# Optimization experiments

Measured on AMD Instinct MI355X. Metric: run time of the kernel, lower is better.

Reference implementation:

```python
import jax, jax.numpy as jnp
import numpy as np

B, N, D, E, FF, K = 2, 1024, 768, 8, 4, 2
H = D * FF  # 3072


def _xavier_uniform(key, shape, gain=1.0):
    # shape is (..., out, in) like torch Linear weight; fan_in/out from last two dims
    fan_out, fan_in = shape[-2], shape[-1]
    limit = gain * np.sqrt(6.0 / (fan_in + fan_out))
    return jax.random.uniform(key, shape, jnp.float32, -limit, limit)


def setup_inputs() -> dict:
    key = jax.random.key(0)
    ks = jax.random.split(key, 5)
    tokens = jax.random.normal(ks[0], (B, N, D), jnp.float32)
    # Token-choice top-K routing: softmax over experts, keep top-K weights
    logits = jax.random.normal(ks[1], (B, N, E), jnp.float32)
    probs = jax.nn.softmax(logits, axis=-1)
    topv, topi = jax.lax.top_k(probs, K)              # (B,N,K)
    onehot = jax.nn.one_hot(topi, E, dtype=jnp.float32)  # (B,N,K,E)
    combine_weights = jnp.einsum('bnk,bnke->bne', topv, onehot)  # (B,N,E)
    dispatch_weights = (combine_weights > 0).astype(jnp.float32)
    # Stacked expert weights (torch Linear convention: W is (out, in), y = x @ W.T)
    Wg = _xavier_uniform(ks[2], (E, H, D))
    Wv = _xavier_uniform(ks[3], (E, H, D))
    Wo = _xavier_uniform(ks[4], (E, D, H), gain=0.02)
    scale = jnp.full((E,), 1.0 / E, jnp.float32)  # output_scale init = 1/E
    return dict(tokens=tokens, dispatch_weights=dispatch_weights,
                combine_weights=combine_weights, Wg=Wg, Wv=Wv, Wo=Wo, scale=scale)


def reference(tokens, dispatch_weights, combine_weights, Wg, Wv, Wo, scale):
    Bb, Nn, Dd = tokens.shape
    Ee = Wg.shape[0]
    x = tokens.reshape(Bb * Nn, Dd)                    # (T, D)
    mask = (dispatch_weights.reshape(-1, Ee) > 0).astype(x.dtype)  # (T, E)
    comb = combine_weights.reshape(-1, Ee) * mask      # zero where not dispatched
    # SwiGLU-style expert FFN, all experts in one grouped contraction
    gate = jax.nn.gelu(jnp.einsum('td,ehd->teh', x, Wg), approximate=False)  # (T,E,H)
    value = jnp.einsum('td,ehd->teh', x, Wv)           # (T,E,H)
    expert_out = jnp.einsum('teh,edh->ted', gate * value, Wo) * scale[None, :, None]  # (T,E,D)
    # Weighted combine: sum_e comb[t,e] * expert_out[t,e,:]
    y = jnp.einsum('ted,te->td', expert_out, comb)     # (T, D)
    return y.reshape(Bb, Nn, Dd)
```

## Files before the change

### kernel.cpp

```cpp
#include <hip/hip_runtime.h>
#include <hip/hip_bf16.h>
#include <math.h>

#define T_TOK 2048
#define DIM   768
#define NEXP  8
#define HDIM  3072
#define MAXP  (T_TOK * 2)
#define LDST  40
#define NTILE_MAX 40

typedef __attribute__((ext_vector_type(8))) short bfrag;
typedef __attribute__((ext_vector_type(4))) float f32x4;

__device__ __forceinline__ unsigned short f2bf(float f) {
  union { float f; unsigned int u; } x; x.f = f;
  unsigned int r = x.u + 0x7fffu + ((x.u >> 16) & 1u);
  return (unsigned short)(r >> 16);
}

__global__ void k_route(const float* __restrict__ disp,
                        const float* __restrict__ comb,
                        int* __restrict__ meta,
                        float* __restrict__ row_comb,
                        int* __restrict__ row_token,
                        int* __restrict__ tok2pair) {
  __shared__ int s_cnt[NEXP], s_off[NEXP], s_cur[NEXP];
  __shared__ int s_tn[T_TOK];
  int tid = threadIdx.x;
  if (tid < NEXP) s_cnt[tid] = 0;
  for (int t = tid; t < T_TOK; t += 256) s_tn[t] = 0;
  __syncthreads();
  for (int t = tid; t < T_TOK; t += 256)
    for (int e = 0; e < NEXP; ++e)
      if (disp[t * NEXP + e] > 0.f) atomicAdd(&s_cnt[e], 1);
  __syncthreads();
  if (tid == 0) {
    int acc = 0;
    for (int e = 0; e < NEXP; ++e) { s_off[e] = acc; acc += s_cnt[e]; }
  }
  __syncthreads();
  if (tid < NEXP) {
    s_cur[tid] = s_off[tid];
    meta[tid] = s_cnt[tid];
    meta[NEXP + tid] = s_off[tid];
  }
  __syncthreads();
  for (int t = tid; t < T_TOK; t += 256)
    for (int e = 0; e < NEXP; ++e)
      if (disp[t * NEXP + e] > 0.f) {
        int p = atomicAdd(&s_cur[e], 1);
        row_token[p] = t;
        row_comb[p] = comb[t * NEXP + e];
        int sl = atomicAdd(&s_tn[t], 1);
        tok2pair[t * 2 + sl] = p;
      }
  __syncthreads();
  if (tid == 0) {
    int nt = 0;
    for (int e = 0; e < NEXP; ++e)
      for (int m0 = 0; m0 < s_cnt[e]; m0 += 128)
        meta[17 + nt++] = (e << 16) | (m0 >> 7);
    meta[16] = nt;
  }
}

__global__ void k_xbf(const float* __restrict__ X, unsigned short* __restrict__ Xb) {
  size_t i = ((size_t)blockIdx.x * 256 + threadIdx.x) * 8;
  float4 a = *(const float4*)(X + i);
  float4 b = *(const float4*)(X + i + 4);
  unsigned short r[8];
  r[0]=f2bf(a.x); r[1]=f2bf(a.y); r[2]=f2bf(a.z); r[3]=f2bf(a.w);
  r[4]=f2bf(b.x); r[5]=f2bf(b.y); r[6]=f2bf(b.z); r[7]=f2bf(b.w);
  *(uint4*)(Xb + i) = *(uint4*)r;
}

__global__ __launch_bounds__(256, 2) void k_gemm_gv(
    const unsigned short* __restrict__ Xb,
    const float* __restrict__ Wg,
    const float* __restrict__ Wv,
    const int* __restrict__ meta,
    const int* __restrict__ row_token,
    unsigned short* __restrict__ ubuf)
{
  int blk = blockIdx.x;
  int c = blk & 7, slot = blk >> 3;
  int nt = c + 8 * (slot / NTILE_MAX);
  int t  = slot % NTILE_MAX;
  if (t >= meta[16]) return;
  int tv = meta[17 + t];
  int e = tv >> 16, m0 = (tv & 0xffff) << 7;
  int cnt = meta[e], off = meta[NEXP + e];
  int n0 = nt * 128;

  __shared__ unsigned short As[128 * LDST];
  __shared__ unsigned short Bgs[128 * LDST];
  __shared__ unsigned short Bvs[128 * LDST];

  int tid = threadIdx.x;
  int wid = tid >> 6, lane = tid & 63;
  int wm = (wid >> 1) * 64, wn = (wid & 1) * 64;
  int lr = lane & 15, quad = lane >> 4;

  int a_tok[2];
#pragma unroll
  for (int r = 0; r < 2; ++r) {
    int row = (tid + 256 * r) >> 2;
    int gr = m0 + row; if (gr >= cnt) gr = cnt - 1;
    a_tok[r] = row_token[off + gr];
  }

  const float* Wgb = Wg + (size_t)e * ((size_t)HDIM * DIM);
  const float* Wvb = Wv + (size_t)e * ((size_t)HDIM * DIM);

  f32x4 zero4 = {0.f, 0.f, 0.f, 0.f};
  f32x4 accg[4][4], accv[4][4];
#pragma unroll
  for (int i = 0; i < 4; ++i)
#pragma unroll
    for (int j = 0; j < 4; ++j) { accg[i][j] = zero4; accv[i][j] = zero4; }

  for (int k0 = 0; k0 < DIM; k0 += 32) {
    __syncthreads();
#pragma unroll
    for (int r = 0; r < 2; ++r) {
      int c2 = tid + 256 * r;
      int row = c2 >> 2, sub = c2 & 3;
      uint4 av = *(const uint4*)(Xb + (size_t)a_tok[r] * DIM + k0 + sub * 8);
      *(uint4*)(&As[row * LDST + sub * 8]) = av;
    }
#pragma unroll
    for (int r = 0; r < 4; ++r) {
      int c2 = tid + 256 * r;
      int row = c2 >> 3, c4 = c2 & 7;
      float4 gv = *(const float4*)(Wgb + (size_t)(n0 + row) * DIM + k0 + c4 * 4);
      ushort4 gp;
      gp.x = f2bf(gv.x); gp.y = f2bf(gv.y); gp.z = f2bf(gv.z); gp.w = f2bf(gv.w);
      *(ushort4*)(&Bgs[row * LDST + c4 * 4]) = gp;
      float4 vv = *(const float4*)(Wvb + (size_t)(n0 + row) * DIM + k0 + c4 * 4);
      ushort4 vp;
      vp.x = f2bf(vv.x); vp.y = f2bf(vv.y); vp.z = f2bf(vv.z); vp.w = f2bf(vv.w);
      *(ushort4*)(&Bvs[row * LDST + c4 * 4]) = vp;
    }
    __syncthreads();
    bfrag a[4], bg[4], bv[4];
#pragma unroll
    for (int i = 0; i < 4; ++i)
      a[i] = *(const bfrag*)(&As[(wm + i * 16 + lr) * LDST + quad * 8]);
#pragma unroll
    for (int j = 0; j < 4; ++j) {
      bg[j] = *(const bfrag*)(&Bgs[(wn + j * 16 + lr) * LDST + quad * 8]);
      bv[j] = *(const bfrag*)(&Bvs[(wn + j * 16 + lr) * LDST + quad * 8]);
    }
#pragma unroll
    for (int i = 0; i < 4; ++i)
#pragma unroll
      for (int j = 0; j < 4; ++j) {
        accg[i][j] = __builtin_amdgcn_mfma_f32_16x16x32_bf16(a[i], bg[j], accg[i][j], 0, 0, 0);
        accv[i][j] = __builtin_amdgcn_mfma_f32_16x16x32_bf16(a[i], bv[j], accv[i][j], 0, 0, 0);
      }
  }

#pragma unroll
  for (int i = 0; i < 4; ++i)
#pragma unroll
    for (int rg = 0; rg < 4; ++rg) {
      int gr = m0 + wm + i * 16 + quad * 4 + rg;
      if (gr < cnt) {
        size_t base = (size_t)(off + gr) * HDIM + n0 + wn;
#pragma unroll
        for (int j = 0; j < 4; ++j) {
          float g = accg[i][j][rg];
          float v = accv[i][j][rg];
          float u = 0.5f * g * (1.0f + erff(g * 0.70710678118654752f)) * v;
          ubuf[base + j * 16 + lr] = f2bf(u);
        }
      }
    }
}

__global__ __launch_bounds__(256, 2) void k_gemm_out(
    const unsigned short* __restrict__ U,
    const float* __restrict__ Wo,
    const float* __restrict__ scale,
    const int* __restrict__ meta,
    const int* __restrict__ row_token,
    const float* __restrict__ row_comb,
    float* __restrict__ partial,
    float* __restrict__ out,
    int mode)
{
  int blk = blockIdx.x;
  int c = blk & 7, slot = blk >> 3;
  int sidx = c + 8 * (slot / NTILE_MAX);
  int nt = sidx % 6, ks = sidx / 6;
  int t = slot % NTILE_MAX;
  if (t >= meta[16]) return;
  int tv = meta[17 + t];
  int e = tv >> 16, m0 = (tv & 0xffff) << 7;
  int cnt = meta[e], off = meta[NEXP + e];
  int n0 = nt * 128;
  int kbase = ks * (HDIM / 4);

  __shared__ unsigned short As[128 * LDST];
  __shared__ unsigned short Bs[128 * LDST];

  int tid = threadIdx.x;
  int wid = tid >> 6, lane = tid & 63;
  int wm = (wid >> 1) * 64, wn = (wid & 1) * 64;
  int lr = lane & 15, quad = lane >> 4;

  int a_grow[2];
#pragma unroll
  for (int r = 0; r < 2; ++r) {
    int row = (tid + 256 * r) >> 2;
    int gr = m0 + row; if (gr >= cnt) gr = cnt - 1;
    a_grow[r] = off + gr;
  }

  const float* Wb = Wo + (size_t)e * ((size_t)DIM * HDIM);

  f32x4 zero4 = {0.f, 0.f, 0.f, 0.f};
  f32x4 acc[4][4];
#pragma unroll
  for (int i = 0; i < 4; ++i)
#pragma unroll
    for (int j = 0; j < 4; ++j) acc[i][j] = zero4;

  for (int kk = 0; kk < HDIM / 4; kk += 32) {
    int k0 = kbase + kk;
    __syncthreads();
#pragma unroll
    for (int r = 0; r < 2; ++r) {
      int c2 = tid + 256 * r;
      int row = c2 >> 2, sub = c2 & 3;
      uint4 av = *(const uint4*)(U + (size_t)a_grow[r] * HDIM + k0 + sub * 8);
      *(uint4*)(&As[row * LDST + sub * 8]) = av;
    }
#pragma unroll
    for (int r = 0; r < 4; ++r) {
      int c2 = tid + 256 * r;
      int row = c2 >> 3, c4 = c2 & 7;
      float4 bvv = *(const float4*)(Wb + (size_t)(n0 + row) * HDIM + k0 + c4 * 4);
      ushort4 bp;
      bp.x = f2bf(bvv.x); bp.y = f2bf(bvv.y); bp.z = f2bf(bvv.z); bp.w = f2bf(bvv.w);
      *(ushort4*)(&Bs[row * LDST + c4 * 4]) = bp;
    }
    __syncthreads();
    bfrag a[4], b[4];
#pragma unroll
    for (int i = 0; i < 4; ++i)
      a[i] = *(const bfrag*)(&As[(wm + i * 16 + lr) * LDST + quad * 8]);
#pragma unroll
    for (int j = 0; j < 4; ++j)
      b[j] = *(const bfrag*)(&Bs[(wn + j * 16 + lr) * LDST + quad * 8]);
#pragma unroll
    for (int i = 0; i < 4; ++i)
#pragma unroll
      for (int j = 0; j < 4; ++j)
        acc[i][j] = __builtin_amdgcn_mfma_f32_16x16x32_bf16(a[i], b[j], acc[i][j], 0, 0, 0);
  }

  float sc = scale[e];
#pragma unroll
  for (int i = 0; i < 4; ++i)
#pragma unroll
    for (int rg = 0; rg < 4; ++rg) {
      int gr = m0 + wm + i * 16 + quad * 4 + rg;
      if (gr < cnt) {
        int grow = off + gr;
        float w = row_comb[grow] * sc;
        if (mode == 0) {
          float* pb = partial + ((size_t)ks * MAXP + grow) * DIM + n0 + wn;
#pragma unroll
          for (int j = 0; j < 4; ++j)
            pb[j * 16 + lr] = acc[i][j][rg] * w;
        } else {
          int tok = row_token[grow];
          float* ob = out + (size_t)tok * DIM + n0 + wn;
#pragma unroll
          for (int j = 0; j < 4; ++j)
            atomicAdd(ob + j * 16 + lr, acc[i][j][rg] * w);
        }
      }
    }
}

__global__ void k_combine(const float* __restrict__ partial,
                          const int* __restrict__ tok2pair,
                          float* __restrict__ out) {
  int idx = blockIdx.x * 256 + threadIdx.x;
  int t = idx / 192, d4 = idx % 192;
  int p0 = tok2pair[t * 2], p1 = tok2pair[t * 2 + 1];
  float sx = 0.f, sy = 0.f, sz = 0.f, sw = 0.f;
#pragma unroll
  for (int ks = 0; ks < 4; ++ks) {
    float4 a = *(const float4*)(partial + ((size_t)ks * MAXP + p0) * DIM + d4 * 4);
    float4 b = *(const float4*)(partial + ((size_t)ks * MAXP + p1) * DIM + d4 * 4);
    sx += a.x + b.x; sy += a.y + b.y; sz += a.z + b.z; sw += a.w + b.w;
  }
  float4 r; r.x = sx; r.y = sy; r.z = sz; r.w = sw;
  *(float4*)(out + (size_t)t * DIM + d4 * 4) = r;
}

extern "C" void kernel_launch(void* const* d_in, const int* in_sizes, int n_in,
                              void* d_out, int out_size, void* d_ws, size_t ws_size,
                              hipStream_t stream) {
  const float* tokens = (const float*)d_in[0];
  const float* disp   = (const float*)d_in[1];
  const float* comb   = (const float*)d_in[2];
  const float* Wg     = (const float*)d_in[3];
  const float* Wv     = (const float*)d_in[4];
  const float* Wo     = (const float*)d_in[5];
  const float* scale  = (const float*)d_in[6];
  float* out = (float*)d_out;

  char* ws = (char*)d_ws;
  int*   meta      = (int*)ws;
  int*   row_token = (int*)(ws + 16384);
  float* row_comb  = (float*)(ws + 32768);
  int*   tok2pair  = (int*)(ws + 49152);
  unsigned short* Xb   = (unsigned short*)(ws + (1u << 20));
  unsigned short* ubuf = (unsigned short*)(ws + (5u << 20));
  float* partial = (float*)(ws + (32ull << 20));
  size_t need_partial = (32ull << 20) + (size_t)4 * MAXP * DIM * sizeof(float);
  int mode = (ws_size >= need_partial) ? 0 : 1;

  hipLaunchKernelGGL(k_route, dim3(1), dim3(256), 0, stream,
                     disp, comb, meta, row_comb, row_token, tok2pair);
  hipLaunchKernelGGL(k_xbf, dim3((T_TOK * DIM) / (256 * 8)), dim3(256), 0, stream,
                     tokens, Xb);
  hipLaunchKernelGGL(k_gemm_gv, dim3(NTILE_MAX * 24), dim3(256), 0, stream,
                     Xb, Wg, Wv, meta, row_token, ubuf);
  if (mode == 1)
    hipMemsetAsync(d_out, 0, (size_t)out_size * sizeof(float), stream);
  hipLaunchKernelGGL(k_gemm_out, dim3(NTILE_MAX * 6 * 4), dim3(256), 0, stream,
                     ubuf, Wo, scale, meta, row_token, row_comb, partial, out, mode);
  if (mode == 0)
    hipLaunchKernelGGL(k_combine, dim3((T_TOK * DIM / 4) / 256), dim3(256), 0, stream,
                       partial, tok2pair, out);
}
```

Measured before the change: 411.0 us.

## Shrink gate/value GEMM M-tile to 64 and register-prefetch next K slice

The gate/value GEMM now uses 64-row token tiles, with its own 64-row tile list built in the routing kernel, so more blocks are launched and the idle padding rows per expert shrink. Both GEMMs now load the next K slice of activations and weights into registers while the current slice is being consumed, which hides global load latency behind the MFMA work. The cost is more register pressure and, for the smaller tile, each fp32 weight tile is reloaded and converted about twice as often.

```diff
diff --git a/kernel.cpp b/kernel.cpp
--- a/kernel.cpp
+++ b/kernel.cpp
@@ -8,7 +8,8 @@
 #define HDIM  3072
 #define MAXP  (T_TOK * 2)
 #define LDST  40
-#define NTILE_MAX 40
+#define NT64_MAX  72
+#define NT128_MAX 40
 
 typedef __attribute__((ext_vector_type(8))) short bfrag;
 typedef __attribute__((ext_vector_type(4))) float f32x4;
@@ -59,9 +60,14 @@
   if (tid == 0) {
     int nt = 0;
     for (int e = 0; e < NEXP; ++e)
+      for (int m0 = 0; m0 < s_cnt[e]; m0 += 64)
+        meta[17 + nt++] = (e << 16) | (m0 >> 6);
+    meta[16] = nt;
+    int nt2 = 0;
+    for (int e = 0; e < NEXP; ++e)
       for (int m0 = 0; m0 < s_cnt[e]; m0 += 128)
-        meta[17 + nt++] = (e << 16) | (m0 >> 7);
-    meta[16] = nt;
+        meta[90 + nt2++] = (e << 16) | (m0 >> 7);
+    meta[89] = nt2;
   }
 }
 
@@ -85,67 +91,77 @@
 {
   int blk = blockIdx.x;
   int c = blk & 7, slot = blk >> 3;
-  int nt = c + 8 * (slot / NTILE_MAX);
-  int t  = slot % NTILE_MAX;
+  int nt = c + 8 * (slot / NT64_MAX);
+  int t  = slot % NT64_MAX;
   if (t >= meta[16]) return;
   int tv = meta[17 + t];
-  int e = tv >> 16, m0 = (tv & 0xffff) << 7;
+  int e = tv >> 16, m0 = (tv & 0xffff) << 6;
   int cnt = meta[e], off = meta[NEXP + e];
   int n0 = nt * 128;
 
-  __shared__ unsigned short As[128 * LDST];
+  __shared__ unsigned short As[64 * LDST];
   __shared__ unsigned short Bgs[128 * LDST];
   __shared__ unsigned short Bvs[128 * LDST];
 
   int tid = threadIdx.x;
   int wid = tid >> 6, lane = tid & 63;
-  int wm = (wid >> 1) * 64, wn = (wid & 1) * 64;
+  int wm = (wid >> 1) * 32, wn = (wid & 1) * 64;
   int lr = lane & 15, quad = lane >> 4;
 
-  int a_tok[2];
-#pragma unroll
-  for (int r = 0; r < 2; ++r) {
-    int row = (tid + 256 * r) >> 2;
-    int gr = m0 + row; if (gr >= cnt) gr = cnt - 1;
-    a_tok[r] = row_token[off + gr];
-  }
+  int arow = tid >> 2, asub = tid & 3;
+  int atok;
+  { int gr = m0 + arow; if (gr >= cnt) gr = cnt - 1;
+    atok = row_token[off + gr]; }
 
   const float* Wgb = Wg + (size_t)e * ((size_t)HDIM * DIM);
   const float* Wvb = Wv + (size_t)e * ((size_t)HDIM * DIM);
 
+  int brow[4], bc4[4];
+#pragma unroll
+  for (int r = 0; r < 4; ++r) { int c2 = tid + 256 * r; brow[r] = c2 >> 3; bc4[r] = c2 & 7; }
+
   f32x4 zero4 = {0.f, 0.f, 0.f, 0.f};
-  f32x4 accg[4][4], accv[4][4];
-#pragma unroll
-  for (int i = 0; i < 4; ++i)
+  f32x4 accg[2][4], accv[2][4];
+#pragma unroll
+  for (int i = 0; i < 2; ++i)
 #pragma unroll
     for (int j = 0; j < 4; ++j) { accg[i][j] = zero4; accv[i][j] = zero4; }
+
+  uint4 aR;
+  float4 gR[4], vR[4];
+
+  aR = *(const uint4*)(Xb + (size_t)atok * DIM + asub * 8);
+#pragma unroll
+  for (int r = 0; r < 4; ++r) {
+    gR[r] = *(const float4*)(Wgb + (size_t)(n0 + brow[r]) * DIM + bc4[r] * 4);
+    vR[r] = *(const float4*)(Wvb + (size_t)(n0 + brow[r]) * DIM + bc4[r] * 4);
+  }
 
   for (int k0 = 0; k0 < DIM; k0 += 32) {
     __syncthreads();
-#pragma unroll
-    for (int r = 0; r < 2; ++r) {
-      int c2 = tid + 256 * r;
-      int row = c2 >> 2, sub = c2 & 3;
-      uint4 av = *(const uint4*)(Xb + (size_t)a_tok[r] * DIM + k0 + sub * 8);
-      *(uint4*)(&As[row * LDST + sub * 8]) = av;
-    }
+    *(uint4*)(&As[arow * LDST + asub * 8]) = aR;
 #pragma unroll
     for (int r = 0; r < 4; ++r) {
-      int c2 = tid + 256 * r;
-      int row = c2 >> 3, c4 = c2 & 7;
-      float4 gv = *(const float4*)(Wgb + (size_t)(n0 + row) * DIM + k0 + c4 * 4);
       ushort4 gp;
-      gp.x = f2bf(gv.x); gp.y = f2bf(gv.y); gp.z = f2bf(gv.z); gp.w = f2bf(gv.w);
-      *(ushort4*)(&Bgs[row * LDST + c4 * 4]) = gp;
-      float4 vv = *(const float4*)(Wvb + (size_t)(n0 + row) * DIM + k0 + c4 * 4);
+      gp.x = f2bf(gR[r].x); gp.y = f2bf(gR[r].y); gp.z = f2bf(gR[r].z); gp.w = f2bf(gR[r].w);
+      *(ushort4*)(&Bgs[brow[r] * LDST + bc4[r] * 4]) = gp;
       ushort4 vp;
-      vp.x = f2bf(vv.x); vp.y = f2bf(vv.y); vp.z = f2bf(vv.z); vp.w = f2bf(vv.w);
-      *(ushort4*)(&Bvs[row * LDST + c4 * 4]) = vp;
+      vp.x = f2bf(vR[r].x); vp.y = f2bf(vR[r].y); vp.z = f2bf(vR[r].z); vp.w = f2bf(vR[r].w);
+      *(ushort4*)(&Bvs[brow[r] * LDST + bc4[r] * 4]) = vp;
+    }
+    int kn = k0 + 32;
+    if (kn < DIM) {
+      aR = *(const uint4*)(Xb + (size_t)atok * DIM + kn + asub * 8);
+#pragma unroll
+      for (int r = 0; r < 4; ++r) {
+        gR[r] = *(const float4*)(Wgb + (size_t)(n0 + brow[r]) * DIM + kn + bc4[r] * 4);
+        vR[r] = *(const float4*)(Wvb + (size_t)(n0 + brow[r]) * DIM + kn + bc4[r] * 4);
+      }
     }
     __syncthreads();
-    bfrag a[4], bg[4], bv[4];
-#pragma unroll
-    for (int i = 0; i < 4; ++i)
+    bfrag a[2], bg[4], bv[4];
+#pragma unroll
+    for (int i = 0; i < 2; ++i)
       a[i] = *(const bfrag*)(&As[(wm + i * 16 + lr) * LDST + quad * 8]);
 #pragma unroll
     for (int j = 0; j < 4; ++j) {
@@ -153,7 +169,7 @@
       bv[j] = *(const bfrag*)(&Bvs[(wn + j * 16 + lr) * LDST + quad * 8]);
     }
 #pragma unroll
-    for (int i = 0; i < 4; ++i)
+    for (int i = 0; i < 2; ++i)
 #pragma unroll
       for (int j = 0; j < 4; ++j) {
         accg[i][j] = __builtin_amdgcn_mfma_f32_16x16x32_bf16(a[i], bg[j], accg[i][j], 0, 0, 0);
@@ -162,7 +178,7 @@
   }
 
 #pragma unroll
-  for (int i = 0; i < 4; ++i)
+  for (int i = 0; i < 2; ++i)
 #pragma unroll
     for (int rg = 0; rg < 4; ++rg) {
       int gr = m0 + wm + i * 16 + quad * 4 + rg;
@@ -192,11 +208,11 @@
 {
   int blk = blockIdx.x;
   int c = blk & 7, slot = blk >> 3;
-  int sidx = c + 8 * (slot / NTILE_MAX);
+  int sidx = c + 8 * (slot / NT128_MAX);
   int nt = sidx % 6, ks = sidx / 6;
-  int t = slot % NTILE_MAX;
-  if (t >= meta[16]) return;
-  int tv = meta[17 + t];
+  int t = slot % NT128_MAX;
+  if (t >= meta[89]) return;
+  int tv = meta[90 + t];
   int e = tv >> 16, m0 = (tv & 0xffff) << 7;
   int cnt = meta[e], off = meta[NEXP + e];
   int n0 = nt * 128;
@@ -217,8 +233,13 @@
     int gr = m0 + row; if (gr >= cnt) gr = cnt - 1;
     a_grow[r] = off + gr;
   }
+  int asub = tid & 3;
 
   const float* Wb = Wo + (size_t)e * ((size_t)DIM * HDIM);
+
+  int brow[4], bc4[4];
+#pragma unroll
+  for (int r = 0; r < 4; ++r) { int c2 = tid + 256 * r; brow[r] = c2 >> 3; bc4[r] = c2 & 7; }
 
   f32x4 zero4 = {0.f, 0.f, 0.f, 0.f};
   f32x4 acc[4][4];
@@ -226,25 +247,39 @@
   for (int i = 0; i < 4; ++i)
 #pragma unroll
     for (int j = 0; j < 4; ++j) acc[i][j] = zero4;
+
+  uint4 aR[2];
+  float4 bR[4];
+
+#pragma unroll
+  for (int r = 0; r < 2; ++r)
+    aR[r] = *(const uint4*)(U + (size_t)a_grow[r] * HDIM + kbase + asub * 8);
+#pragma unroll
+  for (int r = 0; r < 4; ++r)
+    bR[r] = *(const float4*)(Wb + (size_t)(n0 + brow[r]) * HDIM + kbase + bc4[r] * 4);
 
   for (int kk = 0; kk < HDIM / 4; kk += 32) {
     int k0 = kbase + kk;
     __syncthreads();
 #pragma unroll
     for (int r = 0; r < 2; ++r) {
-      int c2 = tid + 256 * r;
-      int row = c2 >> 2, sub = c2 & 3;
-      uint4 av = *(const uint4*)(U + (size_t)a_grow[r] * HDIM + k0 + sub * 8);
-      *(uint4*)(&As[row * LDST + sub * 8]) = av;
+      int row = (tid + 256 * r) >> 2;
+      *(uint4*)(&As[row * LDST + asub * 8]) = aR[r];
     }
 #pragma unroll
     for (int r = 0; r < 4; ++r) {
-      int c2 = tid + 256 * r;
-      int row = c2 >> 3, c4 = c2 & 7;
-      float4 bvv = *(const float4*)(Wb + (size_t)(n0 + row) * HDIM + k0 + c4 * 4);
       ushort4 bp;
-      bp.x = f2bf(bvv.x); bp.y = f2bf(bvv.y); bp.z = f2bf(bvv.z); bp.w = f2bf(bvv.w);
-      *(ushort4*)(&Bs[row * LDST + c4 * 4]) = bp;
+      bp.x = f2bf(bR[r].x); bp.y = f2bf(bR[r].y); bp.z = f2bf(bR[r].z); bp.w = f2bf(bR[r].w);
+      *(ushort4*)(&Bs[brow[r] * LDST + bc4[r] * 4]) = bp;
+    }
+    int kn = k0 + 32;
+    if (kk + 32 < HDIM / 4) {
+#pragma unroll
+      for (int r = 0; r < 2; ++r)
+        aR[r] = *(const uint4*)(U + (size_t)a_grow[r] * HDIM + kn + asub * 8);
+#pragma unroll
+      for (int r = 0; r < 4; ++r)
+        bR[r] = *(const float4*)(Wb + (size_t)(n0 + brow[r]) * HDIM + kn + bc4[r] * 4);
     }
     __syncthreads();
     bfrag a[4], b[4];
@@ -330,11 +365,11 @@
                      disp, comb, meta, row_comb, row_token, tok2pair);
   hipLaunchKernelGGL(k_xbf, dim3((T_TOK * DIM) / (256 * 8)), dim3(256), 0, stream,
                      tokens, Xb);
-  hipLaunchKernelGGL(k_gemm_gv, dim3(NTILE_MAX * 24), dim3(256), 0, stream,
+  hipLaunchKernelGGL(k_gemm_gv, dim3(NT64_MAX * 24), dim3(256), 0, stream,
                      Xb, Wg, Wv, meta, row_token, ubuf);
   if (mode == 1)
     hipMemsetAsync(d_out, 0, (size_t)out_size * sizeof(float), stream);
-  hipLaunchKernelGGL(k_gemm_out, dim3(NTILE_MAX * 6 * 4), dim3(256), 0, stream,
+  hipLaunchKernelGGL(k_gemm_out, dim3(NT128_MAX * 6 * 4), dim3(256), 0, stream,
                      ubuf, Wo, scale, meta, row_token, row_comb, partial, out, mode);
   if (mode == 0)
     hipLaunchKernelGGL(k_combine, dim3((T_TOK * DIM / 4) / 256), dim3(256), 0, stream,
```

Result: slower. 484.9 us (+18.0%).
